# Optimization experiments

Hardware: AMD Instinct MI355X
Metric: run time of the kernel (lower is better)

The kernel has to match this reference:

```python
import jax, jax.numpy as jnp
import numpy as np

# ---- static config (from grid_conf / data_aug_conf) ----
B, N, C = 4, 6, 64            # batch, cameras, camC
OGH, OGW = 256, 704           # final_dim
DOWN = 16                     # 32 // up_scale
FH, FW = OGH // DOWN, OGW // DOWN   # 16, 44
DB0, DB1, DBS = 4.0, 45.0, 1.0      # dbound
D = int((DB1 - DB0) / DBS)          # 41 depth bins
DX = np.array([0.5, 0.5, 20.0], np.float32)            # dx
BX = np.array([-49.75, -49.75, 0.0], np.float32)        # bx (lower + dx/2)
NX = (200, 200, 1)                                       # nx


def make_frustum():
    # [D, FH, FW, 3] pixel (u, v, depth) frustum, matches torch create_frustum
    ds = jnp.arange(DB0, DB1, DBS, dtype=jnp.float32)[:, None, None] * jnp.ones((1, FH, FW), jnp.float32)
    xs = jnp.linspace(0.0, OGW - 1.0, FW, dtype=jnp.float32)[None, None, :] * jnp.ones((D, FH, 1), jnp.float32)
    ys = jnp.linspace(0.0, OGH - 1.0, FH, dtype=jnp.float32)[None, :, None] * jnp.ones((D, 1, FW), jnp.float32)
    return jnp.stack([xs, ys, ds], axis=-1)


def get_geometry(rots, trans, intrins, post_rots, post_trans):
    # frustum points -> ego frame, [B, N, D, FH, FW, 3]
    pts = make_frustum()[None, None] - post_trans[:, :, None, None, None, :]
    pts = jnp.einsum('bnij,bndhwj->bndhwi', jnp.linalg.inv(post_rots), pts)
    # un-project: (u*d, v*d, d)
    pts = jnp.concatenate([pts[..., :2] * pts[..., 2:3], pts[..., 2:3]], axis=-1)
    combine = rots @ jnp.linalg.inv(intrins)
    return jnp.einsum('bnij,bndhwj->bndhwi', combine, pts) + trans[:, :, None, None, None, :]


def voxel_pooling(geom, x):
    # geom: [B,N,D,H,W,3] ego coords; x: [B,N,D,H,W,C] lifted features
    dx = jnp.asarray(DX); bx = jnp.asarray(BX)
    # voxel indices; .astype(int32) truncates toward zero like torch .long()
    gi = ((geom - (bx - dx / 2.0)) / dx).astype(jnp.int32)
    Np = B * N * D * FH * FW
    gi = gi.reshape(Np, 3)
    xf = x.reshape(Np, C)
    bidx = jnp.repeat(jnp.arange(B, dtype=jnp.int32), N * D * FH * FW)
    valid = ((gi[:, 0] >= 0) & (gi[:, 0] < NX[0]) &
             (gi[:, 1] >= 0) & (gi[:, 1] < NX[1]) &
             (gi[:, 2] >= 0) & (gi[:, 2] < NX[2]))
    # flat voxel id: (((b*nz + z)*nx0 + xi)*nx1 + yi)
    flat = ((bidx * NX[2] + gi[:, 2]) * NX[0] + gi[:, 0]) * NX[1] + gi[:, 1]
    flat = jnp.where(valid, flat, 0)
    xf = xf * valid[:, None].astype(xf.dtype)
    nvox = B * NX[2] * NX[0] * NX[1]
    # scatter-add == sort + cumsum-trick per-voxel sum in the torch code
    final = jax.ops.segment_sum(xf, flat, num_segments=nvox)          # [nvox, C]
    final = final.reshape(B, NX[2], NX[0], NX[1], C)
    final = jnp.transpose(final, (0, 1, 4, 2, 3)).reshape(B, NX[2] * C, NX[0], NX[1])
    return final


def setup_inputs() -> dict:
    key = jax.random.key(0)
    k1, k2 = jax.random.split(key)
    feat_depth = jax.random.normal(k1, (B, N, D, FH, FW), jnp.float32)
    feat_pv = jax.random.normal(k2, (B, N, C, FH, FW), jnp.float32)
    # realistic 6-camera nuScenes-like rig, intrinsics scaled to 704x256
    base = np.array([[0., 0., 1.], [-1., 0., 0.], [0., -1., 0.]], np.float32)  # cam axes -> ego axes
    rots = np.zeros((B, N, 3, 3), np.float32)
    trans = np.zeros((B, N, 3), np.float32)
    for n in range(N):
        yaw = 2.0 * np.pi * n / N
        Rz = np.array([[np.cos(yaw), -np.sin(yaw), 0.], [np.sin(yaw), np.cos(yaw), 0.], [0., 0., 1.]], np.float32)
        rots[:, n] = Rz @ base
        trans[:, n] = Rz @ np.array([1.5, 0.0, 1.6], np.float32)
    fx = 1266.0 * (OGW / 1600.0)
    intr = np.array([[fx, 0., OGW / 2.0], [0., fx, OGH / 2.0], [0., 0., 1.]], np.float32)
    return {
        'feat_depth': feat_depth,
        'feat_pv': feat_pv,
        'rots': jnp.asarray(rots),
        'trans': jnp.asarray(trans),
        'intrins': jnp.asarray(np.broadcast_to(intr, (B, N, 3, 3)).copy()),
        'post_rots': jnp.asarray(np.broadcast_to(np.eye(3, dtype=np.float32), (B, N, 3, 3)).copy()),
        'post_trans': jnp.zeros((B, N, 3), jnp.float32),
    }


def reference(feat_depth, feat_pv, rots, trans, intrins, post_rots, post_trans):
    geom = get_geometry(rots, trans, intrins, post_rots, post_trans)
    geom = jax.lax.stop_gradient(geom)  # torch casts to .long(): indices are non-diff
    depth = jax.nn.softmax(feat_depth, axis=2)                 # get_depth_dist over D
    # lift: depth.unsqueeze(1) * feat.unsqueeze(2) -> [B,N,D,C,H,W] -> [B,N,D,H,W,C]
    x = depth[:, :, :, None] * feat_pv[:, :, None]
    x = jnp.transpose(x, (0, 1, 2, 4, 5, 3))
    return voxel_pooling(geom, x)                               # [B, C*nz, 200, 200]
```

## Files before the change

kernel.cpp:

```cpp
#include <hip/hip_runtime.h>
#include <math.h>

namespace {
constexpr int kB = 4, kN = 6, kC = 64, kD = 41, kFH = 16, kFW = 44;
constexpr int kNX0 = 200, kNX1 = 200;
constexpr int kHW  = kFH * kFW;
constexpr int kPix = kB * kN * kHW;
constexpr int kPts = kPix * kD;
constexpr int kVox = kB * kNX0 * kNX1;
constexpr int kPvElems = kPix * kC;
constexpr int kScanBlks = kVox / 256;
constexpr int kPvtTiles = kPix / 64;
constexpr int kSmBlks = kPix / 256;
constexpr int kFrontBlks = kPvtTiles + kSmBlks + kScanBlks;

constexpr size_t kOffPvT    = 0;
constexpr size_t kSzPvT     = (size_t)kPvElems * 4;
constexpr size_t kOffVox    = kOffPvT + kSzPvT;
constexpr size_t kSzVox     = (size_t)kPts * 4;
constexpr size_t kOffWgt    = kOffVox + kSzVox;
constexpr size_t kSzWgt     = (size_t)kPts * 4;
constexpr size_t kOffCnt    = kOffWgt + kSzWgt;
constexpr size_t kSzCnt     = (size_t)kVox * 4;
constexpr size_t kOffOffs   = kOffCnt + kSzCnt;
constexpr size_t kSzOffs    = 640256;
constexpr size_t kOffBSum   = kOffOffs + kSzOffs;
constexpr size_t kSzBSum    = 2560;
constexpr size_t kOffSKW    = kOffBSum + kSzBSum;
constexpr size_t kSzSKW     = (size_t)kPts * 8;
constexpr size_t kWsNeed    = kOffSKW + kSzSKW + 256;
}

__device__ __forceinline__ void inv3x3(const float m[9], float inv[9]) {
    float a = m[0], b = m[1], c = m[2];
    float d = m[3], e = m[4], f = m[5];
    float g = m[6], h = m[7], i = m[8];
    float A =  (e * i - f * h);
    float Bm = -(d * i - f * g);
    float Cm =  (d * h - e * g);
    float det = a * A + b * Bm + c * Cm;
    float r = 1.0f / det;
    inv[0] = A * r;
    inv[1] = -(b * i - c * h) * r;
    inv[2] =  (b * f - c * e) * r;
    inv[3] = Bm * r;
    inv[4] =  (a * i - c * g) * r;
    inv[5] = -(a * f - c * d) * r;
    inv[6] = Cm * r;
    inv[7] = -(a * h - b * g) * r;
    inv[8] =  (a * e - b * d) * r;
}

__device__ __forceinline__ int geo_flat(int q,
                                        const float* __restrict__ rots,
                                        const float* __restrict__ trans,
                                        const float* __restrict__ intrins,
                                        const float* __restrict__ post_rots,
                                        const float* __restrict__ post_trans) {
    const int bn  = q / (kD * kHW);
    const int rem = q - bn * (kD * kHW);
    const int d   = rem / kHW;
    const int hw  = rem - d * kHW;
    const int h   = hw / kFW;
    const int w   = hw - h * kFW;
    const int b   = bn / kN;

    const float* R  = rots       + bn * 9;
    const float* K  = intrins    + bn * 9;
    const float* PR = post_rots  + bn * 9;
    const float* PT = post_trans + bn * 3;
    const float* T  = trans      + bn * 3;

    float Km[9], PRm[9];
#pragma unroll
    for (int i = 0; i < 9; ++i) { Km[i] = K[i]; PRm[i] = PR[i]; }
    float invK[9], invPR[9];
    inv3x3(Km, invK);
    inv3x3(PRm, invPR);
    float M[9];
#pragma unroll
    for (int i = 0; i < 3; ++i)
#pragma unroll
        for (int j = 0; j < 3; ++j)
            M[i * 3 + j] = R[i * 3 + 0] * invK[0 * 3 + j]
                         + R[i * 3 + 1] * invK[1 * 3 + j]
                         + R[i * 3 + 2] * invK[2 * 3 + j];

    const float u  = (float)w * (703.0f / 43.0f);
    const float v  = (float)h * 17.0f;
    const float dv = 4.0f + (float)d;
    const float px = u - PT[0], py = v - PT[1], pz = dv - PT[2];
    const float ax = invPR[0] * px + invPR[1] * py + invPR[2] * pz;
    const float ay = invPR[3] * px + invPR[4] * py + invPR[5] * pz;
    const float az = invPR[6] * px + invPR[7] * py + invPR[8] * pz;
    const float qx = ax * az, qy = ay * az, qz = az;
    const float gx = M[0] * qx + M[1] * qy + M[2] * qz + T[0];
    const float gy = M[3] * qx + M[4] * qy + M[5] * qz + T[1];
    const float gz = M[6] * qx + M[7] * qy + M[8] * qz + T[2];
    const float fx = (gx + 50.0f) / 0.5f;
    const float fy = (gy + 50.0f) / 0.5f;
    const float fz = (gz + 10.0f) / 20.0f;
    const int gix = (int)fx;
    const int giy = (int)fy;
    const int giz = (int)fz;
    if (gix >= 0 && gix < kNX0 && giy >= 0 && giy < kNX1 && giz == 0)
        return (b * kNX0 + gix) * kNX1 + giy;
    return -1;
}

__global__ __launch_bounds__(256) void lss_front(const float* __restrict__ pv,
                                                 const float* __restrict__ feat_depth,
                                                 float* __restrict__ pvT,
                                                 float* __restrict__ wgtArr,
                                                 unsigned* __restrict__ counts) {
    __shared__ float t[64][65];
    const int blk = blockIdx.x;
    const int tid = threadIdx.x;

    if (blk < kPvtTiles) {
        const int pix0 = blk * 64;
        const int bn  = pix0 / kHW;
        const int hw0 = pix0 - bn * kHW;
        const int lane = tid & 63;
        const int wv   = tid >> 6;
        const float* src = pv + (size_t)(bn * kC) * kHW + hw0;
#pragma unroll
        for (int cc = 0; cc < 16; ++cc) {
            const int c = wv * 16 + cc;
            t[c][lane] = src[(size_t)c * kHW + lane];
        }
        __syncthreads();
        float* dst = pvT + (size_t)pix0 * kC;
#pragma unroll
        for (int jj = 0; jj < 16; ++jj) {
            const int j = wv * 16 + jj;
            dst[j * kC + lane] = t[lane][j];
        }
    } else if (blk < kPvtTiles + kSmBlks) {
        const int pix = (blk - kPvtTiles) * 256 + tid;
        const int bn = pix / kHW;
        const int hw = pix - bn * kHW;
        const float* p = feat_depth + (size_t)(bn * kD) * kHW + hw;
        float v[kD];
#pragma unroll
        for (int d = 0; d < kD; ++d) v[d] = p[(size_t)d * kHW];
        float mx = v[0];
#pragma unroll
        for (int d = 1; d < kD; ++d) mx = fmaxf(mx, v[d]);
        float sm = 0.0f;
#pragma unroll
        for (int d = 0; d < kD; ++d) { v[d] = __expf(v[d] - mx); sm += v[d]; }
        const float inv = 1.0f / sm;
        float* o = wgtArr + (size_t)(bn * kD) * kHW + hw;
#pragma unroll
        for (int d = 0; d < kD; ++d) o[(size_t)d * kHW] = v[d] * inv;
    } else {
        const int ci = (blk - kPvtTiles - kSmBlks) * 256 + tid;
        counts[ci] = 0u;
    }
}

__global__ __launch_bounds__(256) void lss_geo(
    const float* __restrict__ rots,
    const float* __restrict__ trans,
    const float* __restrict__ intrins,
    const float* __restrict__ post_rots,
    const float* __restrict__ post_trans,
    int* __restrict__ voxArr,
    unsigned* __restrict__ counts)
{
    const int q = blockIdx.x * 256 + threadIdx.x;
    const int f = geo_flat(q, rots, trans, intrins, post_rots, post_trans);
    if (f >= 0) atomicAdd(&counts[f], 1u);
    voxArr[q] = f;
}

__global__ __launch_bounds__(256) void lss_scan_a(const unsigned* __restrict__ counts,
                                                  unsigned* __restrict__ offsets,
                                                  unsigned* __restrict__ blockSums) {
    const int i = blockIdx.x * 256 + threadIdx.x;
    const int lane = threadIdx.x & 63;
    const int wv = threadIdx.x >> 6;
    const unsigned c = counts[i];
    unsigned s = c;
#pragma unroll
    for (int o = 1; o < 64; o <<= 1) {
        unsigned v = __shfl_up(s, o);
        if (lane >= o) s += v;
    }
    __shared__ unsigned wsum[4];
    if (lane == 63) wsum[wv] = s;
    __syncthreads();
    unsigned base = 0;
#pragma unroll
    for (int k = 0; k < 3; ++k)
        if (k < wv) base += wsum[k];
    const unsigned incl = s + base;
    offsets[i] = incl - c;
    if (threadIdx.x == 255) blockSums[blockIdx.x] = incl;
}

__global__ __launch_bounds__(1024) void lss_scan_b(unsigned* __restrict__ blockSums) {
    const int t = threadIdx.x;
    const int lane = t & 63;
    const int wv = t >> 6;
    const unsigned c = (t < kScanBlks) ? blockSums[t] : 0u;
    unsigned s = c;
#pragma unroll
    for (int o = 1; o < 64; o <<= 1) {
        unsigned v = __shfl_up(s, o);
        if (lane >= o) s += v;
    }
    __shared__ unsigned wsum[16];
    if (lane == 63) wsum[wv] = s;
    __syncthreads();
    unsigned base = 0;
#pragma unroll
    for (int k = 0; k < 15; ++k)
        if (k < wv) base += wsum[k];
    if (t < kScanBlks) blockSums[t] = (s + base) - c;
}

__global__ __launch_bounds__(256) void lss_order(const int* __restrict__ voxArr,
                                                 const float* __restrict__ wgtArr,
                                                 unsigned* __restrict__ offsets,
                                                 const unsigned* __restrict__ blockSums,
                                                 uint2* __restrict__ skw) {
    const int q = blockIdx.x * 256 + threadIdx.x;
    const int f = voxArr[q];
    if (f >= 0) {
        const unsigned slot = atomicAdd(&offsets[f], 1u) + blockSums[f >> 8];
        const int bn  = q / (kD * kHW);
        const int rem = q - bn * (kD * kHW);
        const int hw  = rem % kHW;
        uint2 u;
        u.x = (unsigned)(bn * kHW + hw);
        u.y = __float_as_uint(wgtArr[q]);
        skw[slot] = u;
    }
}

__global__ __launch_bounds__(512) void lss_gather(const float* __restrict__ pvT,
                                                  const unsigned* __restrict__ offsets,
                                                  const unsigned* __restrict__ blockSums,
                                                  const uint2* __restrict__ skw,
                                                  float* __restrict__ out) {
    constexpr int kChunk = 2048;
    __shared__ float acc[50][65];
    __shared__ uint2 sbuf[kChunk];
    __shared__ unsigned rowOff[51];
    const int tile = blockIdx.x;
    const int yt = tile & 3;
    const int xi = (tile >> 2) % kNX0;
    const int b  = tile / (kNX0 * 4);
    const int yi0 = yt * 50;
    const int lane = threadIdx.x & 63;
    const int wave = threadIdx.x >> 6;
    const int flat0 = (b * kNX0 + xi) * kNX1 + yi0;

    for (int e = threadIdx.x; e < 50 * 65; e += 512)
        ((float*)acc)[e] = 0.0f;
    if (threadIdx.x < 51) {
        const int f = flat0 - 1 + (int)threadIdx.x;
        rowOff[threadIdx.x] = (f < 0) ? 0u : (offsets[f] + blockSums[f >> 8]);
    }
    __syncthreads();

    const unsigned seg0 = rowOff[0];
    const unsigned seg1 = rowOff[50];

    for (unsigned cb = seg0; cb < seg1; cb += (unsigned)kChunk) {
        const unsigned ce = min(cb + (unsigned)kChunk, seg1);
        const int n = (int)(ce - cb);
        for (int e = threadIdx.x; e < n; e += 512)
            sbuf[e] = skw[cb + e];
        __syncthreads();

        for (int j = wave; j < 50; j += 8) {
            unsigned s0 = max(rowOff[j], cb);
            unsigned e0 = min(rowOff[j + 1], ce);
            if (s0 >= e0) continue;
            float a0 = 0.0f, a1 = 0.0f, a2 = 0.0f, a3 = 0.0f;
            int p  = (int)(s0 - cb);
            int pe = (int)(e0 - cb);
            for (; p + 8 <= pe; p += 8) {
                const uint2 u0 = sbuf[p + 0];
                const uint2 u1 = sbuf[p + 1];
                const uint2 u2 = sbuf[p + 2];
                const uint2 u3 = sbuf[p + 3];
                const uint2 u4 = sbuf[p + 4];
                const uint2 u5 = sbuf[p + 5];
                const uint2 u6 = sbuf[p + 6];
                const uint2 u7 = sbuf[p + 7];
                const float* r0 = pvT + (size_t)((unsigned)__builtin_amdgcn_readfirstlane(u0.x)) * kC;
                const float* r1 = pvT + (size_t)((unsigned)__builtin_amdgcn_readfirstlane(u1.x)) * kC;
                const float* r2 = pvT + (size_t)((unsigned)__builtin_amdgcn_readfirstlane(u2.x)) * kC;
                const float* r3 = pvT + (size_t)((unsigned)__builtin_amdgcn_readfirstlane(u3.x)) * kC;
                const float* r4 = pvT + (size_t)((unsigned)__builtin_amdgcn_readfirstlane(u4.x)) * kC;
                const float* r5 = pvT + (size_t)((unsigned)__builtin_amdgcn_readfirstlane(u5.x)) * kC;
                const float* r6 = pvT + (size_t)((unsigned)__builtin_amdgcn_readfirstlane(u6.x)) * kC;
                const float* r7 = pvT + (size_t)((unsigned)__builtin_amdgcn_readfirstlane(u7.x)) * kC;
                const float f0 = r0[lane], f1 = r1[lane], f2 = r2[lane], f3 = r3[lane];
                const float f4 = r4[lane], f5 = r5[lane], f6 = r6[lane], f7 = r7[lane];
                a0 = fmaf(__uint_as_float(__builtin_amdgcn_readfirstlane(u0.y)), f0, a0);
                a1 = fmaf(__uint_as_float(__builtin_amdgcn_readfirstlane(u1.y)), f1, a1);
                a2 = fmaf(__uint_as_float(__builtin_amdgcn_readfirstlane(u2.y)), f2, a2);
                a3 = fmaf(__uint_as_float(__builtin_amdgcn_readfirstlane(u3.y)), f3, a3);
                a0 = fmaf(__uint_as_float(__builtin_amdgcn_readfirstlane(u4.y)), f4, a0);
                a1 = fmaf(__uint_as_float(__builtin_amdgcn_readfirstlane(u5.y)), f5, a1);
                a2 = fmaf(__uint_as_float(__builtin_amdgcn_readfirstlane(u6.y)), f6, a2);
                a3 = fmaf(__uint_as_float(__builtin_amdgcn_readfirstlane(u7.y)), f7, a3);
            }
            for (; p < pe; ++p) {
                const uint2 u = sbuf[p];
                const float* r = pvT + (size_t)((unsigned)__builtin_amdgcn_readfirstlane(u.x)) * kC;
                a0 = fmaf(__uint_as_float(__builtin_amdgcn_readfirstlane(u.y)), r[lane], a0);
            }
            acc[j][lane] += (a0 + a1) + (a2 + a3);
        }
        __syncthreads();
    }
    __syncthreads();

    for (int e = threadIdx.x; e < kC * 50; e += 512) {
        const int c = e / 50, j = e % 50;
        out[((b * kC + c) * (kNX0 * kNX1)) + xi * kNX1 + yi0 + j] = acc[j][c];
    }
}

__global__ __launch_bounds__(256) void lss_scatter_fb(
    const float* __restrict__ feat_depth,
    const float* __restrict__ feat_pv,
    const float* __restrict__ rots,
    const float* __restrict__ trans,
    const float* __restrict__ intrins,
    const float* __restrict__ post_rots,
    const float* __restrict__ post_trans,
    float* __restrict__ out)
{
    const int lane = threadIdx.x & 63;
    const int wave = threadIdx.x >> 6;
    const int pix  = blockIdx.x * 4 + wave;
    const int w  = pix % kFW;
    const int h  = (pix / kFW) % kFH;
    const int bn = pix / kHW;
    const int b  = bn / kN;
    const int pixBase = h * kFW + w;
    float fd = -INFINITY;
    if (lane < kD)
        fd = feat_depth[(bn * kD + lane) * kHW + pixBase];
    float mx = fd;
#pragma unroll
    for (int off = 32; off >= 1; off >>= 1)
        mx = fmaxf(mx, __shfl_xor(mx, off));
    float ex = (lane < kD) ? __expf(fd - mx) : 0.0f;
    float sm = ex;
#pragma unroll
    for (int off = 32; off >= 1; off >>= 1)
        sm += __shfl_xor(sm, off);
    const float wgt = ex / sm;
    int vox = -1;
    if (lane < kD) {
        const int q = (bn * kD + lane) * kHW + pixBase;
        const int f = geo_flat(q, rots, trans, intrins, post_rots, post_trans);
        if (f >= 0) vox = f % (kNX0 * kNX1);
    }
    const float fc = feat_pv[(bn * kC + lane) * kHW + pixBase];
    const int outBase = (b * kC + lane) * (kNX0 * kNX1);
#pragma unroll 1
    for (int d = 0; d < kD; ++d) {
        const int   vd = __shfl(vox, d);
        const float wd = __shfl(wgt, d);
        if (vd >= 0)
            atomicAdd(&out[outBase + vd], wd * fc);
    }
}

extern "C" void kernel_launch(void* const* d_in, const int* in_sizes, int n_in,
                              void* d_out, int out_size, void* d_ws, size_t ws_size,
                              hipStream_t stream) {
    const float* feat_depth = (const float*)d_in[0];
    const float* feat_pv    = (const float*)d_in[1];
    const float* rots       = (const float*)d_in[2];
    const float* trans      = (const float*)d_in[3];
    const float* intrins    = (const float*)d_in[4];
    const float* post_rots  = (const float*)d_in[5];
    const float* post_trans = (const float*)d_in[6];
    float* out = (float*)d_out;

    if (ws_size < kWsNeed) {
        hipMemsetAsync(out, 0, (size_t)out_size * sizeof(float), stream);
        lss_scatter_fb<<<kPix / 4, 256, 0, stream>>>(
            feat_depth, feat_pv, rots, trans, intrins, post_rots, post_trans, out);
        return;
    }

    char* ws = (char*)d_ws;
    float*    pvT      = (float*)   (ws + kOffPvT);
    int*      voxArr   = (int*)     (ws + kOffVox);
    float*    wgtArr   = (float*)   (ws + kOffWgt);
    unsigned* counts   = (unsigned*)(ws + kOffCnt);
    unsigned* offsets  = (unsigned*)(ws + kOffOffs);
    unsigned* blockSums= (unsigned*)(ws + kOffBSum);
    uint2*    skw      = (uint2*)   (ws + kOffSKW);

    lss_front<<<kFrontBlks, 256, 0, stream>>>(feat_pv, feat_depth, pvT, wgtArr, counts);
    lss_geo<<<kPts / 256, 256, 0, stream>>>(
        rots, trans, intrins, post_rots, post_trans, voxArr, counts);
    lss_scan_a<<<kScanBlks, 256, 0, stream>>>(counts, offsets, blockSums);
    lss_scan_b<<<1, 1024, 0, stream>>>(blockSums);
    lss_order<<<kPts / 256, 256, 0, stream>>>(voxArr, wgtArr, offsets, blockSums, skw);
    lss_gather<<<kB * kNX0 * 4, 512, 0, stream>>>(pvT, offsets, blockSums, skw, out);
}
```

Before: 112.1 us.

## Fuse two-pass scan via last-block ticket and recompute voxel ids instead of storing

The separate block-sum scan kernel is folded into the first scan kernel: each block publishes its sum, and the last block to take an atomic ticket scans all block sums into a new bases array. The per-point voxel id array is dropped, and lss_order recomputes the geometry per point instead of reading it back. This removes one kernel launch and a write plus a read of a per-point int array, at the cost of duplicated geometry math and a serial tail in the last scan block.

Measured after the change: 130.2 us. 16.2% more time.

```diff
diff --git a/kernel.cpp b/kernel.cpp
--- a/kernel.cpp
+++ b/kernel.cpp
@@ -16,9 +16,7 @@
 
 constexpr size_t kOffPvT    = 0;
 constexpr size_t kSzPvT     = (size_t)kPvElems * 4;
-constexpr size_t kOffVox    = kOffPvT + kSzPvT;
-constexpr size_t kSzVox     = (size_t)kPts * 4;
-constexpr size_t kOffWgt    = kOffVox + kSzVox;
+constexpr size_t kOffWgt    = kOffPvT + kSzPvT;
 constexpr size_t kSzWgt     = (size_t)kPts * 4;
 constexpr size_t kOffCnt    = kOffWgt + kSzWgt;
 constexpr size_t kSzCnt     = (size_t)kVox * 4;
@@ -26,7 +24,11 @@
 constexpr size_t kSzOffs    = 640256;
 constexpr size_t kOffBSum   = kOffOffs + kSzOffs;
 constexpr size_t kSzBSum    = 2560;
-constexpr size_t kOffSKW    = kOffBSum + kSzBSum;
+constexpr size_t kOffBase   = kOffBSum + kSzBSum;
+constexpr size_t kSzBase    = 2560;
+constexpr size_t kOffTick   = kOffBase + kSzBase;
+constexpr size_t kSzTick    = 256;
+constexpr size_t kOffSKW    = kOffTick + kSzTick;
 constexpr size_t kSzSKW     = (size_t)kPts * 8;
 constexpr size_t kWsNeed    = kOffSKW + kSzSKW + 256;
 }
@@ -112,10 +114,12 @@
                                                  const float* __restrict__ feat_depth,
                                                  float* __restrict__ pvT,
                                                  float* __restrict__ wgtArr,
-                                                 unsigned* __restrict__ counts) {
+                                                 unsigned* __restrict__ counts,
+                                                 unsigned* __restrict__ ticket) {
     __shared__ float t[64][65];
     const int blk = blockIdx.x;
     const int tid = threadIdx.x;
+    if (blk == 0 && tid == 0) *ticket = 0u;
 
     if (blk < kPvtTiles) {
         const int pix0 = blk * 64;
@@ -166,21 +170,25 @@
     const float* __restrict__ intrins,
     const float* __restrict__ post_rots,
     const float* __restrict__ post_trans,
-    int* __restrict__ voxArr,
     unsigned* __restrict__ counts)
 {
     const int q = blockIdx.x * 256 + threadIdx.x;
     const int f = geo_flat(q, rots, trans, intrins, post_rots, post_trans);
     if (f >= 0) atomicAdd(&counts[f], 1u);
-    voxArr[q] = f;
-}
-
-__global__ __launch_bounds__(256) void lss_scan_a(const unsigned* __restrict__ counts,
-                                                  unsigned* __restrict__ offsets,
-                                                  unsigned* __restrict__ blockSums) {
-    const int i = blockIdx.x * 256 + threadIdx.x;
-    const int lane = threadIdx.x & 63;
-    const int wv = threadIdx.x >> 6;
+}
+
+__global__ __launch_bounds__(256) void lss_scan(const unsigned* __restrict__ counts,
+                                                unsigned* __restrict__ offsets,
+                                                unsigned* __restrict__ blockSums,
+                                                unsigned* __restrict__ bases,
+                                                unsigned* __restrict__ ticket) {
+    __shared__ unsigned wsum[4];
+    __shared__ int lastFlag;
+    const int tid = threadIdx.x;
+    const int i = blockIdx.x * 256 + tid;
+    const int lane = tid & 63;
+    const int wv = tid >> 6;
+
     const unsigned c = counts[i];
     unsigned s = c;
 #pragma unroll
@@ -188,7 +196,6 @@
         unsigned v = __shfl_up(s, o);
         if (lane >= o) s += v;
     }
-    __shared__ unsigned wsum[4];
     if (lane == 63) wsum[wv] = s;
     __syncthreads();
     unsigned base = 0;
@@ -197,39 +204,56 @@
         if (k < wv) base += wsum[k];
     const unsigned incl = s + base;
     offsets[i] = incl - c;
-    if (threadIdx.x == 255) blockSums[blockIdx.x] = incl;
-}
-
-__global__ __launch_bounds__(1024) void lss_scan_b(unsigned* __restrict__ blockSums) {
-    const int t = threadIdx.x;
-    const int lane = t & 63;
-    const int wv = t >> 6;
-    const unsigned c = (t < kScanBlks) ? blockSums[t] : 0u;
-    unsigned s = c;
+    if (tid == 255) {
+        atomicExch(&blockSums[blockIdx.x], incl);
+        __threadfence();
+    }
+    __syncthreads();
+    if (tid == 0)
+        lastFlag = (atomicAdd(ticket, 1u) == (unsigned)(kScanBlks - 1));
+    __syncthreads();
+    if (!lastFlag) return;
+
+    __threadfence();
+    const int lo = tid * 3;
+    const unsigned c0 = (lo     < kScanBlks) ? blockSums[lo]     : 0u;
+    const unsigned c1 = (lo + 1 < kScanBlks) ? blockSums[lo + 1] : 0u;
+    const unsigned c2 = (lo + 2 < kScanBlks) ? blockSums[lo + 2] : 0u;
+    const unsigned t3 = c0 + c1 + c2;
+    unsigned si = t3;
 #pragma unroll
     for (int o = 1; o < 64; o <<= 1) {
-        unsigned v = __shfl_up(s, o);
-        if (lane >= o) s += v;
-    }
-    __shared__ unsigned wsum[16];
-    if (lane == 63) wsum[wv] = s;
-    __syncthreads();
-    unsigned base = 0;
-#pragma unroll
-    for (int k = 0; k < 15; ++k)
-        if (k < wv) base += wsum[k];
-    if (t < kScanBlks) blockSums[t] = (s + base) - c;
-}
-
-__global__ __launch_bounds__(256) void lss_order(const int* __restrict__ voxArr,
-                                                 const float* __restrict__ wgtArr,
-                                                 unsigned* __restrict__ offsets,
-                                                 const unsigned* __restrict__ blockSums,
-                                                 uint2* __restrict__ skw) {
+        unsigned v = __shfl_up(si, o);
+        if (lane >= o) si += v;
+    }
+    __syncthreads();
+    if (lane == 63) wsum[wv] = si;
+    __syncthreads();
+    unsigned b2 = 0;
+#pragma unroll
+    for (int k = 0; k < 3; ++k)
+        if (k < wv) b2 += wsum[k];
+    unsigned run = si - t3 + b2;
+    if (lo     < kScanBlks) { bases[lo]     = run; run += c0; }
+    if (lo + 1 < kScanBlks) { bases[lo + 1] = run; run += c1; }
+    if (lo + 2 < kScanBlks) { bases[lo + 2] = run; run += c2; }
+}
+
+__global__ __launch_bounds__(256) void lss_order(
+    const float* __restrict__ rots,
+    const float* __restrict__ trans,
+    const float* __restrict__ intrins,
+    const float* __restrict__ post_rots,
+    const float* __restrict__ post_trans,
+    const float* __restrict__ wgtArr,
+    unsigned* __restrict__ offsets,
+    const unsigned* __restrict__ bases,
+    uint2* __restrict__ skw)
+{
     const int q = blockIdx.x * 256 + threadIdx.x;
-    const int f = voxArr[q];
+    const int f = geo_flat(q, rots, trans, intrins, post_rots, post_trans);
     if (f >= 0) {
-        const unsigned slot = atomicAdd(&offsets[f], 1u) + blockSums[f >> 8];
+        const unsigned slot = atomicAdd(&offsets[f], 1u) + bases[f >> 8];
         const int bn  = q / (kD * kHW);
         const int rem = q - bn * (kD * kHW);
         const int hw  = rem % kHW;
@@ -242,7 +266,7 @@
 
 __global__ __launch_bounds__(512) void lss_gather(const float* __restrict__ pvT,
                                                   const unsigned* __restrict__ offsets,
-                                                  const unsigned* __restrict__ blockSums,
+                                                  const unsigned* __restrict__ bases,
                                                   const uint2* __restrict__ skw,
                                                   float* __restrict__ out) {
     constexpr int kChunk = 2048;
@@ -262,7 +286,7 @@
         ((float*)acc)[e] = 0.0f;
     if (threadIdx.x < 51) {
         const int f = flat0 - 1 + (int)threadIdx.x;
-        rowOff[threadIdx.x] = (f < 0) ? 0u : (offsets[f] + blockSums[f >> 8]);
+        rowOff[threadIdx.x] = (f < 0) ? 0u : (offsets[f] + bases[f >> 8]);
     }
     __syncthreads();
 
@@ -397,18 +421,20 @@
 
     char* ws = (char*)d_ws;
     float*    pvT      = (float*)   (ws + kOffPvT);
-    int*      voxArr   = (int*)     (ws + kOffVox);
     float*    wgtArr   = (float*)   (ws + kOffWgt);
     unsigned* counts   = (unsigned*)(ws + kOffCnt);
     unsigned* offsets  = (unsigned*)(ws + kOffOffs);
     unsigned* blockSums= (unsigned*)(ws + kOffBSum);
+    unsigned* bases    = (unsigned*)(ws + kOffBase);
+    unsigned* ticket   = (unsigned*)(ws + kOffTick);
     uint2*    skw      = (uint2*)   (ws + kOffSKW);
 
-    lss_front<<<kFrontBlks, 256, 0, stream>>>(feat_pv, feat_depth, pvT, wgtArr, counts);
+    lss_front<<<kFrontBlks, 256, 0, stream>>>(feat_pv, feat_depth, pvT, wgtArr,
+                                              counts, ticket);
     lss_geo<<<kPts / 256, 256, 0, stream>>>(
-        rots, trans, intrins, post_rots, post_trans, voxArr, counts);
-    lss_scan_a<<<kScanBlks, 256, 0, stream>>>(counts, offsets, blockSums);
-    lss_scan_b<<<1, 1024, 0, stream>>>(blockSums);
-    lss_order<<<kPts / 256, 256, 0, stream>>>(voxArr, wgtArr, offsets, blockSums, skw);
-    lss_gather<<<kB * kNX0 * 4, 512, 0, stream>>>(pvT, offsets, blockSums, skw, out);
-}
+        rots, trans, intrins, post_rots, post_trans, counts);
+    lss_scan<<<kScanBlks, 256, 0, stream>>>(counts, offsets, blockSums, bases, ticket);
+    lss_order<<<kPts / 256, 256, 0, stream>>>(
+        rots, trans, intrins, post_rots, post_trans, wgtArr, offsets, bases, skw);
+    lss_gather<<<kB * kNX0 * 4, 512, 0, stream>>>(pvT, offsets, bases, skw, out);
+}
```
